# Kernel optimization log

Measured on AMD Instinct MI355X. Metric: run time of the kernel, lower is better.

Reference implementation:

```python
import jax, jax.numpy as jnp
import numpy as np

K_MAX = 32
IN_DIM = 2
L_NP = np.ones(IN_DIM, dtype=np.float64)
CONTROL_ENERGY_REG = 1e-3


def _density_constants():
    """Replicates Ergodicity_Loss.compute_fourier_coefficients_density (uniform density)."""
    ks = np.arange(K_MAX, dtype=np.float64)
    P, Q = np.meshgrid(ks, ks, indexing='ij')
    kgrid = np.stack([P, Q], axis=-1)                 # [K,K,2] integer modes
    ksc = kgrid * (np.pi / L_NP)                      # scaled modes k*pi/L
    # Lambda_k = (1 + |k|^2)^(-(d+1)/2)
    norm_weights = (1.0 + (ksc ** 2).sum(-1)) ** (-(IN_DIM + 1) / 2.0)
    # h_k: FAITHFUL to the original buggy loop (normal is reset every iteration,
    # so it depends only on the last dimension's index)
    norm_factors = np.where(kgrid[..., -1] == 0, 1.0, np.sqrt(L_NP[-1] / 2.0))
    # characteristic function of uniform density on [0,L1]x...x[0,Ld], real part
    coeff = np.ones((K_MAX, K_MAX), dtype=np.complex128)
    for i in range(IN_DIM):
        ki = ksc[..., i]
        safe = np.where(ki == 0.0, 1.0, ki)
        integral = np.where(ki == 0.0, L_NP[i],
                            (np.exp(1j * ki * L_NP[i]) - 1.0) / (1j * safe))
        coeff *= integral / L_NP[i]
    coeffs_density = coeff.real / norm_factors
    return (coeffs_density.astype(np.float32),
            norm_factors.astype(np.float32),
            norm_weights.astype(np.float32))


def setup_inputs() -> dict:
    key = jax.random.key(0)
    k1, k2 = jax.random.split(key)
    T, B, N = 512, 32, 64
    # agent trajectories in [0,L]^d
    x = jax.random.uniform(k1, (T, B, N, IN_DIM), dtype=jnp.float32)
    # control signals
    u = jax.random.normal(k2, (T, B, N, IN_DIM), dtype=jnp.float32)
    cd, nf, nw = _density_constants()
    return {
        "x": x,
        "u": u,
        "L": jnp.asarray(L_NP, dtype=jnp.float32),
        "coeffs_density": jnp.asarray(cd),
        "norm_factors": jnp.asarray(nf),
        "norm_weights": jnp.asarray(nw),
    }


def reference(x, u, L, coeffs_density, norm_factors, norm_weights):
    T, B, N, d = x.shape                      # d == 2
    K = coeffs_density.shape[0]
    # per-dimension mode frequencies k*pi/L_i  -> [d, K]
    freq = jnp.arange(K, dtype=x.dtype)[None, :] * (jnp.pi / L[:, None])
    c0 = jnp.cos(x[..., 0, None] * freq[0])   # [T,B,N,K]
    c1 = jnp.cos(x[..., 1, None] * freq[1])   # [T,B,N,K]
    # prod over dims then sum over time t and agents n, fused: [B,K,K]
    S = jnp.einsum('tbnp,tbnq->bpq', c0, c1)
    coeffs = S / (norm_factors * (N * T))     # c_k per batch element
    loss = (((coeffs - coeffs_density) ** 2) * norm_weights).sum()
    # control energy regularizer: |u|^2 summed
    loss = loss + CONTROL_ENERGY_REG * (u ** 2).sum() / (2 * N * T * B)
    return loss
```

## Files before the change

### kernel.cpp

```cpp
#include <hip/hip_runtime.h>


#define T_DIM 512
#define B_DIM 32
#define N_DIM 64
#define K_DIM 32
#define TN_TOT (T_DIM * N_DIM)
#define CHUNKS 16
#define NBLK1 (B_DIM * CHUNKS)
#define CHUNK_S (TN_TOT / CHUNKS)
#define TILE_S 512
#define N_TILES (CHUNK_S / TILE_S)
#define ST_PAD (TILE_S + 8)

typedef __attribute__((ext_vector_type(8))) short bf16x8;
typedef __attribute__((ext_vector_type(16))) float f32x16;

__device__ __forceinline__ unsigned pkbf(float a, float b) {
#if __has_builtin(__builtin_amdgcn_cvt_pk_bf16_f32)
  typedef __attribute__((ext_vector_type(2))) __bf16 bf16x2;
  bf16x2 v = __builtin_amdgcn_cvt_pk_bf16_f32(a, b);
  return __builtin_bit_cast(unsigned, v);
#else
  unsigned ua = __float_as_uint(a), ub = __float_as_uint(b);
  ua = (ua + 0x7FFFu + ((ua >> 16) & 1u)) >> 16;
  ub = (ub + 0x7FFFu + ((ub >> 16) & 1u)) >> 16;
  return (ua & 0xFFFFu) | (ub << 16);
#endif
}

__global__ __launch_bounds__(256, 2) void ergo_main(
    const float* __restrict__ x, const float* __restrict__ u,
    const float* __restrict__ L, float* __restrict__ Spart,
    float* __restrict__ u2p, float* __restrict__ loss_acc,
    unsigned* __restrict__ counter) {
  __shared__ alignas(16) unsigned short c0T[K_DIM][ST_PAD];
  __shared__ alignas(16) unsigned short c1T[K_DIM][ST_PAD];
  __shared__ float sred[K_DIM * K_DIM];
  __shared__ float ured[4];

  const int tid = threadIdx.x;
  const int lane = tid & 63;
  const int wave = tid >> 6;
  const int bid = blockIdx.x;
  const int b = bid >> 4;
  const int chunk = bid & (CHUNKS - 1);

  if (bid == 0 && tid == 0) {
    *loss_acc = 0.0f;
    *counter = 0u;
  }

  const float invL0 = 1.0f / L[0];
  const float invL1 = 1.0f / L[1];

  f32x16 acc;
#pragma unroll
  for (int r = 0; r < 16; ++r) acc[r] = 0.0f;
  float usum = 0.0f;

  const int s_base = chunk * CHUNK_S;

  for (int tile = 0; tile < N_TILES; ++tile) {
    const int s0 = s_base + tile * TILE_S;

    {
      const int ls = tid * 2;
      const int s = s0 + ls;
      const int t = s >> 6, n = s & 63;
      const size_t gidx = (((size_t)t * B_DIM + b) * N_DIM + n) * 2;
      const float4 xv = *reinterpret_cast<const float4*>(x + gidx);
      const float4 uv = *reinterpret_cast<const float4*>(u + gidx);
      usum += uv.x * uv.x + uv.y * uv.y + uv.z * uv.z + uv.w * uv.w;

      const float c00 = cospif(xv.x * invL0);
      const float c01 = cospif(xv.y * invL1);
      const float c10 = cospif(xv.z * invL0);
      const float c11 = cospif(xv.w * invL1);

      *reinterpret_cast<unsigned*>(&c0T[0][ls]) = 0x3F803F80u;
      *reinterpret_cast<unsigned*>(&c1T[0][ls]) = 0x3F803F80u;
      *reinterpret_cast<unsigned*>(&c0T[1][ls]) = pkbf(c00, c10);
      *reinterpret_cast<unsigned*>(&c1T[1][ls]) = pkbf(c01, c11);

      float p0 = 1.f, q0 = c00, p1 = 1.f, q1 = c01;
      float p2 = 1.f, q2 = c10, p3 = 1.f, q3 = c11;
      const float t0 = 2.f * c00, t1 = 2.f * c01, t2 = 2.f * c10, t3 = 2.f * c11;
#pragma unroll
      for (int k = 2; k < K_DIM; ++k) {
        const float n0 = __builtin_fmaf(t0, q0, -p0);
        const float n1 = __builtin_fmaf(t1, q1, -p1);
        const float n2 = __builtin_fmaf(t2, q2, -p2);
        const float n3 = __builtin_fmaf(t3, q3, -p3);
        p0 = q0; q0 = n0; p1 = q1; q1 = n1;
        p2 = q2; q2 = n2; p3 = q3; q3 = n3;
        *reinterpret_cast<unsigned*>(&c0T[k][ls]) = pkbf(n0, n2);
        *reinterpret_cast<unsigned*>(&c1T[k][ls]) = pkbf(n1, n3);
      }
    }
    __syncthreads();

    {
      const int p = lane & 31;
      const int sb = wave * 128 + ((lane >> 5) << 3);
      const unsigned short* ar = &c0T[p][sb];
      const unsigned short* br = &c1T[p][sb];
#pragma unroll
      for (int j = 0; j < 8; ++j) {
        const bf16x8 av = *reinterpret_cast<const bf16x8*>(ar + j * 16);
        const bf16x8 bv = *reinterpret_cast<const bf16x8*>(br + j * 16);
        acc = __builtin_amdgcn_mfma_f32_32x32x16_bf16(av, bv, acc, 0, 0, 0);
      }
    }
    __syncthreads();
  }

  for (int i = tid; i < K_DIM * K_DIM; i += 256) sred[i] = 0.0f;
  __syncthreads();
  {
    const int col = lane & 31;
    const int rb = (lane >> 5) * 4;
#pragma unroll
    for (int r = 0; r < 16; ++r) {
      const int row = (r & 3) + 8 * (r >> 2) + rb;
      atomicAdd(&sred[row * 32 + col], acc[r]);
    }
  }
#pragma unroll
  for (int off = 32; off; off >>= 1) usum += __shfl_down(usum, off);
  if (lane == 0) ured[wave] = usum;
  __syncthreads();
  {
    float* dst = Spart + (size_t)bid * (K_DIM * K_DIM);
#pragma unroll
    for (int j = 0; j < 4; ++j) dst[tid + j * 256] = sred[tid + j * 256];
  }
  if (tid == 0) u2p[bid] = ured[0] + ured[1] + ured[2] + ured[3];
}

__global__ __launch_bounds__(256) void ergo_reduce(
    const float* __restrict__ Spart, const float* __restrict__ u2p,
    const float* __restrict__ cd, const float* __restrict__ nf,
    const float* __restrict__ nw, float* __restrict__ loss_acc,
    unsigned* __restrict__ counter, float* __restrict__ out) {
  const int b = blockIdx.x;
  const int tid = threadIdx.x;
  const int lane = tid & 63, wave = tid >> 6;
  __shared__ float red[4];
  __shared__ int winner;

  float sum = 0.0f;
#pragma unroll
  for (int j = 0; j < 4; ++j) {
    const int i = tid + j * 256;
    float s = 0.0f;
#pragma unroll
    for (int c = 0; c < CHUNKS; ++c)
      s += Spart[((size_t)(b * CHUNKS + c)) * (K_DIM * K_DIM) + i];
    const float coeff = s * (1.0f / (float)(N_DIM * T_DIM)) / nf[i];
    const float d = coeff - cd[i];
    sum += d * d * nw[i];
  }
#pragma unroll
  for (int off = 32; off; off >>= 1) sum += __shfl_down(sum, off);
  if (lane == 0) red[wave] = sum;
  __syncthreads();
  if (tid == 0) {
    atomicAdd(loss_acc, red[0] + red[1] + red[2] + red[3]);
    __threadfence();
    const unsigned tk = atomicAdd(counter, 1u);
    winner = (tk == B_DIM - 1) ? 1 : 0;
  }
  __syncthreads();
  if (winner) {
    float us = u2p[tid] + u2p[tid + 256];
#pragma unroll
    for (int off = 32; off; off >>= 1) us += __shfl_down(us, off);
    if (lane == 0) red[wave] = us;
    __syncthreads();
    if (tid == 0) {
      const float u2tot = red[0] + red[1] + red[2] + red[3];
      const float loss = atomicAdd(loss_acc, 0.0f);
      out[0] = loss + u2tot * (1.0e-3f / 2097152.0f);
    }
  }
}

extern "C" void kernel_launch(void* const* d_in, const int* in_sizes, int n_in,
                              void* d_out, int out_size, void* d_ws, size_t ws_size,
                              hipStream_t stream) {
  const float* x = (const float*)d_in[0];
  const float* u = (const float*)d_in[1];
  const float* L = (const float*)d_in[2];
  const float* cd = (const float*)d_in[3];
  const float* nf = (const float*)d_in[4];
  const float* nw = (const float*)d_in[5];

  float* Spart = (float*)d_ws;
  float* u2p = Spart + (size_t)NBLK1 * K_DIM * K_DIM;
  float* loss_acc = u2p + NBLK1;
  unsigned* counter = (unsigned*)(loss_acc + 1);

  ergo_main<<<dim3(NBLK1), dim3(256), 0, stream>>>(x, u, L, Spart, u2p,
                                                   loss_acc, counter);
  ergo_reduce<<<dim3(B_DIM), dim3(256), 0, stream>>>(Spart, u2p, cd, nf, nw,
                                                     loss_acc, counter,
                                                     (float*)d_out);
}
```

Measured before the change: 99.11 us.

## Double chunk count, halve tile size, one sample per thread with fast cosine

Splits each batch into 32 chunks instead of 16 and makes each thread handle one sample per tile instead of two. This doubles the grid to 1024 blocks and raises the occupancy hint to 4 blocks per CU, so more waves are available to hide latency. It also swaps cospif for __cosf on a pi-scaled argument, which is cheaper but less accurate. The cost is twice as many partial sums for the reduce kernel to read, narrower global loads, 16-bit LDS stores in place of packed 32-bit ones, and less MFMA work per synchronisation.

After: 108.2 us. +9.2%, slower.

```diff
diff --git a/kernel.cpp b/kernel.cpp
--- a/kernel.cpp
+++ b/kernel.cpp
@@ -6,12 +6,13 @@
 #define N_DIM 64
 #define K_DIM 32
 #define TN_TOT (T_DIM * N_DIM)
-#define CHUNKS 16
+#define CHUNKS 32
 #define NBLK1 (B_DIM * CHUNKS)
 #define CHUNK_S (TN_TOT / CHUNKS)
-#define TILE_S 512
+#define TILE_S 256
 #define N_TILES (CHUNK_S / TILE_S)
 #define ST_PAD (TILE_S + 8)
+#define U2SCALE (1.0e-3f / 2097152.0f)
 
 typedef __attribute__((ext_vector_type(8))) short bf16x8;
 typedef __attribute__((ext_vector_type(16))) float f32x16;
@@ -29,7 +30,7 @@
 #endif
 }
 
-__global__ __launch_bounds__(256, 2) void ergo_main(
+__global__ __launch_bounds__(256, 4) void ergo_main(
     const float* __restrict__ x, const float* __restrict__ u,
     const float* __restrict__ L, float* __restrict__ Spart,
     float* __restrict__ u2p, float* __restrict__ loss_acc,
@@ -43,7 +44,7 @@
   const int lane = tid & 63;
   const int wave = tid >> 6;
   const int bid = blockIdx.x;
-  const int b = bid >> 4;
+  const int b = bid >> 5;
   const int chunk = bid & (CHUNKS - 1);
 
   if (bid == 0 && tid == 0) {
@@ -51,8 +52,8 @@
     *counter = 0u;
   }
 
-  const float invL0 = 1.0f / L[0];
-  const float invL1 = 1.0f / L[1];
+  const float w0 = 3.14159265358979f / L[0];
+  const float w1 = 3.14159265358979f / L[1];
 
   f32x16 acc;
 #pragma unroll
@@ -65,48 +66,42 @@
     const int s0 = s_base + tile * TILE_S;
 
     {
-      const int ls = tid * 2;
-      const int s = s0 + ls;
+      const int s = s0 + tid;
       const int t = s >> 6, n = s & 63;
       const size_t gidx = (((size_t)t * B_DIM + b) * N_DIM + n) * 2;
-      const float4 xv = *reinterpret_cast<const float4*>(x + gidx);
-      const float4 uv = *reinterpret_cast<const float4*>(u + gidx);
-      usum += uv.x * uv.x + uv.y * uv.y + uv.z * uv.z + uv.w * uv.w;
-
-      const float c00 = cospif(xv.x * invL0);
-      const float c01 = cospif(xv.y * invL1);
-      const float c10 = cospif(xv.z * invL0);
-      const float c11 = cospif(xv.w * invL1);
-
-      *reinterpret_cast<unsigned*>(&c0T[0][ls]) = 0x3F803F80u;
-      *reinterpret_cast<unsigned*>(&c1T[0][ls]) = 0x3F803F80u;
-      *reinterpret_cast<unsigned*>(&c0T[1][ls]) = pkbf(c00, c10);
-      *reinterpret_cast<unsigned*>(&c1T[1][ls]) = pkbf(c01, c11);
-
-      float p0 = 1.f, q0 = c00, p1 = 1.f, q1 = c01;
-      float p2 = 1.f, q2 = c10, p3 = 1.f, q3 = c11;
-      const float t0 = 2.f * c00, t1 = 2.f * c01, t2 = 2.f * c10, t3 = 2.f * c11;
+      const float2 xv = *reinterpret_cast<const float2*>(x + gidx);
+      const float2 uv = *reinterpret_cast<const float2*>(u + gidx);
+      usum += uv.x * uv.x + uv.y * uv.y;
+
+      const float c0 = __cosf(xv.x * w0);
+      const float c1 = __cosf(xv.y * w1);
+
+      c0T[0][tid] = 0x3F80u;
+      c1T[0][tid] = 0x3F80u;
+      c0T[1][tid] = (unsigned short)pkbf(c0, c0);
+      c1T[1][tid] = (unsigned short)pkbf(c1, c1);
+
+      float p0 = 1.f, q0 = c0, p1 = 1.f, q1 = c1;
+      const float t0 = 2.f * c0, t1 = 2.f * c1;
 #pragma unroll
       for (int k = 2; k < K_DIM; ++k) {
         const float n0 = __builtin_fmaf(t0, q0, -p0);
         const float n1 = __builtin_fmaf(t1, q1, -p1);
-        const float n2 = __builtin_fmaf(t2, q2, -p2);
-        const float n3 = __builtin_fmaf(t3, q3, -p3);
-        p0 = q0; q0 = n0; p1 = q1; q1 = n1;
-        p2 = q2; q2 = n2; p3 = q3; q3 = n3;
-        *reinterpret_cast<unsigned*>(&c0T[k][ls]) = pkbf(n0, n2);
-        *reinterpret_cast<unsigned*>(&c1T[k][ls]) = pkbf(n1, n3);
+        p0 = q0; q0 = n0;
+        p1 = q1; q1 = n1;
+        c0T[k][tid] = (unsigned short)pkbf(n0, n0);
+        c1T[k][tid] = (unsigned short)pkbf(n1, n1);
       }
     }
     __syncthreads();
 
     {
       const int p = lane & 31;
-      const int sb = wave * 128 + ((lane >> 5) << 3);
+      const int sb = wave * 64 + ((lane >> 5) << 3);
       const unsigned short* ar = &c0T[p][sb];
       const unsigned short* br = &c1T[p][sb];
 #pragma unroll
-      for (int j = 0; j < 8; ++j) {
+      for (int j = 0; j < 4; ++j) {
         const bf16x8 av = *reinterpret_cast<const bf16x8*>(ar + j * 16);
         const bf16x8 bv = *reinterpret_cast<const bf16x8*>(br + j * 16);
         acc = __builtin_amdgcn_mfma_f32_32x32x16_bf16(av, bv, acc, 0, 0, 0);
@@ -173,7 +168,7 @@
   }
   __syncthreads();
   if (winner) {
-    float us = u2p[tid] + u2p[tid + 256];
+    float us = u2p[tid] + u2p[tid + 256] + u2p[tid + 512] + u2p[tid + 768];
 #pragma unroll
     for (int off = 32; off; off >>= 1) us += __shfl_down(us, off);
     if (lane == 0) red[wave] = us;
@@ -181,7 +176,7 @@
     if (tid == 0) {
       const float u2tot = red[0] + red[1] + red[2] + red[3];
       const float loss = atomicAdd(loss_acc, 0.0f);
-      out[0] = loss + u2tot * (1.0e-3f / 2097152.0f);
+      out[0] = loss + u2tot * U2SCALE;
     }
   }
 }
```
